# Kernel optimization log

Measured on AMD Instinct MI355X. Metric: run time of the kernel, lower is better.

Reference implementation:

```python
import jax, jax.numpy as jnp
import numpy as np

TAU = 0.7
# Dellar moment flip under x<->y swap: (rho, jy, jx, Pyy, Pxy, Pxx, N, Jy, Jx)
FLIP = np.array([0, 2, 1, 5, 4, 3, 6, 8, 7])


def _dellar_matrices():
    # D2Q9 velocities in lettuce stencil order
    e = np.array([[0, 0], [1, 0], [0, 1], [-1, 0], [0, -1],
                  [1, 1], [-1, 1], [-1, -1], [1, -1]], dtype=np.float64)
    ex, ey = e[:, 0], e[:, 1]
    g = np.array([1, -2, -2, -2, -2, 4, 4, 4, 4], dtype=np.float64)  # Dellar ghost mode
    third = 1.0 / 3.0
    M = np.stack([
        np.ones(9),            # rho
        ex,                    # jx
        ey,                    # jy
        ex * ex - third,       # Pxx - cs^2 rho
        ex * ey,               # Pxy
        ey * ey - third,       # Pyy - cs^2 rho
        g,                     # N (ghost)
        g * ex,                # Jx (ghost)
        g * ey,                # Jy (ghost)
    ])
    return M, np.linalg.inv(M)


def _mlp(x, w1, b1, w2, b2):
    # x: (nx, ny, 9) -> (nx, ny, 1); Linear(9,24) + ReLU + Linear(24,1)
    h = jax.nn.relu(jnp.einsum('xyi,oi->xyo', x, w1) + b1)
    return jnp.einsum('xyo,po->xyp', h, w2) + b2


def setup_inputs() -> dict:
    key = jax.random.key(0)
    ks = jax.random.split(key, 9)
    nx = ny = 2048
    f = jax.random.uniform(ks[0], (9, nx, ny), dtype=jnp.float32)

    def lin_w(k, o, i):
        return jax.random.uniform(k, (o, i), dtype=jnp.float32,
                                  minval=-1.0, maxval=1.0) / np.sqrt(i)

    def lin_b(k, o, i):
        return jax.random.uniform(k, (o,), dtype=jnp.float32,
                                  minval=-1.0, maxval=1.0) / np.sqrt(i)

    M, Minv = _dellar_matrices()
    return {
        'f': f,
        'j_w1': lin_w(ks[1], 24, 9), 'j_b1': lin_b(ks[2], 24, 9),
        'j_w2': lin_w(ks[3], 1, 24), 'j_b2': lin_b(ks[4], 1, 24),
        'n_w1': lin_w(ks[5], 24, 9), 'n_b1': lin_b(ks[6], 24, 9),
        'n_w2': lin_w(ks[7], 1, 24), 'n_b2': lin_b(ks[8], 1, 24),
        'M': jnp.asarray(M, jnp.float32),
        'Minv': jnp.asarray(Minv, jnp.float32),
    }


def reference(f, j_w1, j_b1, j_w2, j_b2, n_w1, n_b1, n_w2, n_b2, M, Minv):
    # moment transform: m_i = M_ij f_j, shape (9, nx, ny)
    m = jnp.einsum('ij,jxy->ixy', M, f)
    mt = jnp.transpose(m, (1, 2, 0))        # (nx, ny, 9)
    mtf = mt[..., FLIP]                     # x<->y flipped moments

    gt_half = lambda a: 0.5 + jnp.exp(a)
    tau_jx = gt_half(_mlp(mt, j_w1, j_b1, j_w2, j_b2))[..., 0]
    tau_jy = gt_half(_mlp(mtf, j_w1, j_b1, j_w2, j_b2))[..., 0]
    tau_n = gt_half(_mlp(mt, n_w1, n_b1, n_w2, n_b2)
                    + _mlp(mtf, n_w1, n_b1, n_w2, n_b2))[..., 0]

    taus = jnp.full_like(m, TAU)
    taus = taus.at[6].set(tau_n).at[7].set(tau_jx).at[8].set(tau_jy)

    rho, jx, jy = m[0], m[1], m[2]
    zero = jnp.zeros_like(rho)
    meq = jnp.stack([rho, jx, jy,
                     jx * jx / rho, jx * jy / rho, jy * jy / rho,
                     zero, zero, zero])

    m_post = m - (m - meq) / taus
    return jnp.einsum('ij,jxy->ixy', Minv, m_post)
```

## Files before the change

### kernel.cpp

```cpp
#include <hip/hip_runtime.h>

typedef float f32x2 __attribute__((ext_vector_type(2)));

__device__ __forceinline__ f32x2 splat2(float s) { f32x2 v; v.x = s; v.y = s; return v; }
__device__ __forceinline__ f32x2 pfmas(float a, f32x2 b, f32x2 c) { return __builtin_elementwise_fma(splat2(a), b, c); }
__device__ __forceinline__ f32x2 prelu(f32x2 a) { return __builtin_elementwise_max(a, splat2(0.0f)); }


__global__ __launch_bounds__(256) void prep_kernel(
    const float* __restrict__ j_w1, const float* __restrict__ j_b1,
    const float* __restrict__ j_w2, const float* __restrict__ j_b2,
    const float* __restrict__ n_w1, const float* __restrict__ n_b1,
    const float* __restrict__ n_w2, const float* __restrict__ n_b2,
    const float* __restrict__ Mg, const float* __restrict__ Minvg,
    float* __restrict__ ws)
{
    const int t = threadIdx.x;
    if (t < 48) {
        const int o = t >> 1, which = t & 1;
        const float* w1 = which ? n_w1 : j_w1;
        const float* b1 = which ? n_b1 : j_b1;
        float w[9];
        #pragma unroll
        for (int i = 0; i < 9; ++i) w[i] = w1[o * 9 + i];
        float* dst = ws + o * 24 + which * 10;
        dst[0] = w[0]; dst[1] = w[4]; dst[2] = w[6];
        dst[3] = 0.5f * (w[1] + w[2]); dst[4] = 0.5f * (w[3] + w[5]); dst[5] = 0.5f * (w[7] + w[8]);
        dst[6] = 0.5f * (w[1] - w[2]); dst[7] = 0.5f * (w[3] - w[5]); dst[8] = 0.5f * (w[7] - w[8]);
        dst[9] = b1[o];
        if (!which) {
            ws[o * 24 + 20] = j_w2[o];
            ws[o * 24 + 21] = n_w2[o];
            ws[o * 24 + 22] = 0.0f;
            ws[o * 24 + 23] = 0.0f;
        }
    } else if (t >= 64 && t < 64 + 81) {
        const int e = t - 64, r = e / 9, i = e % 9;
        float v;
        switch (r) {
            case 0: v = Mg[0 * 9 + i]; break;
            case 1: v = Mg[4 * 9 + i]; break;
            case 2: v = Mg[6 * 9 + i]; break;
            case 3: v = Mg[1 * 9 + i] + Mg[2 * 9 + i]; break;
            case 4: v = Mg[3 * 9 + i] + Mg[5 * 9 + i]; break;
            case 5: v = Mg[7 * 9 + i] + Mg[8 * 9 + i]; break;
            case 6: v = Mg[1 * 9 + i] - Mg[2 * 9 + i]; break;
            case 7: v = Mg[3 * 9 + i] - Mg[5 * 9 + i]; break;
            default: v = Mg[7 * 9 + i] - Mg[8 * 9 + i]; break;
        }
        ws[576 + r * 9 + i] = v;
    } else if (t >= 160 && t < 160 + 54) {
        const int e = t - 160, r = e / 6, c = e % 6;
        ws[672 + e] = -Minvg[r * 9 + 3 + c];
    } else if (t == 254) {
        ws[728] = j_b2[0];
    } else if (t == 255) {
        ws[729] = n_b2[0];
    }
}

__global__ __launch_bounds__(256) void mrt_main(
    const float* __restrict__ f, const float* __restrict__ W,
    float* __restrict__ out, int n2)
{
    long base = ((long)blockIdx.x * 256 + threadIdx.x) * 4;
    if (base + 4 > n2) base = n2 - 4;

    f32x2 fv[2][9];
    f32x2 tv[2][9];
    #pragma unroll
    for (int i = 0; i < 9; ++i) {
        const float4 v = *reinterpret_cast<const float4*>(f + (size_t)i * n2 + base);
        fv[0][i].x = v.x; fv[0][i].y = v.y;
        fv[1][i].x = v.z; fv[1][i].y = v.w;
    }
    #pragma unroll
    for (int r = 0; r < 9; ++r) { tv[0][r] = splat2(0.f); tv[1][r] = splat2(0.f); }
    #pragma unroll
    for (int i = 0; i < 9; ++i) {
        #pragma unroll
        for (int r = 0; r < 9; ++r) {
            const float w = W[576 + r * 9 + i];
            tv[0][r] = pfmas(w, fv[0][i], tv[0][r]);
            tv[1][r] = pfmas(w, fv[1][i], tv[1][r]);
        }
    }

    f32x2 accj[2], accjf[2], accn[2];
    #pragma unroll
    for (int p = 0; p < 2; ++p) { accj[p] = splat2(0.f); accjf[p] = splat2(0.f); accn[p] = splat2(0.f); }

    #pragma unroll 4
    for (int o = 0; o < 24; ++o) {
        const float* wo = W + o * 24;
        const float w0 = wo[0], w1 = wo[1], w2 = wo[2], w3 = wo[3], w4 = wo[4], w5 = wo[5];
        const float a0 = wo[6], a1 = wo[7], a2 = wo[8], b1j = wo[9];
        const float u0 = wo[10], u1 = wo[11], u2 = wo[12], u3 = wo[13], u4 = wo[14], u5 = wo[15];
        const float v0 = wo[16], v1 = wo[17], v2 = wo[18], b1n = wo[19];
        const float w2j = wo[20], w2n = wo[21];
        #pragma unroll
        for (int p = 0; p < 2; ++p) {
            f32x2 s = splat2(b1j);
            s = pfmas(w0, tv[p][0], s);
            s = pfmas(w1, tv[p][1], s);
            s = pfmas(w2, tv[p][2], s);
            s = pfmas(w3, tv[p][3], s);
            s = pfmas(w4, tv[p][4], s);
            s = pfmas(w5, tv[p][5], s);
            f32x2 a = splat2(a0) * tv[p][6];
            a = pfmas(a1, tv[p][7], a);
            a = pfmas(a2, tv[p][8], a);
            accj[p]  = pfmas(w2j, prelu(s + a), accj[p]);
            accjf[p] = pfmas(w2j, prelu(s - a), accjf[p]);

            f32x2 sn = splat2(b1n);
            sn = pfmas(u0, tv[p][0], sn);
            sn = pfmas(u1, tv[p][1], sn);
            sn = pfmas(u2, tv[p][2], sn);
            sn = pfmas(u3, tv[p][3], sn);
            sn = pfmas(u4, tv[p][4], sn);
            sn = pfmas(u5, tv[p][5], sn);
            f32x2 an = splat2(v0) * tv[p][6];
            an = pfmas(v1, tv[p][7], an);
            an = pfmas(v2, tv[p][8], an);
            accn[p] = pfmas(w2n, prelu(sn + an) + prelu(sn - an), accn[p]);
        }
    }

    const float b2j = W[728], b2n = W[729];
    f32x2 d[2][6];
    #pragma unroll
    for (int p = 0; p < 2; ++p) {
        const f32x2 aj  = accj[p]  + splat2(b2j);
        const f32x2 ajf = accjf[p] + splat2(b2j);
        const f32x2 an  = accn[p]  + splat2(2.0f * b2n);
        f32x2 rt7, rt8, rt6, rrho;
        rt7.x = __builtin_amdgcn_rcpf(0.5f + __expf(aj.x));
        rt7.y = __builtin_amdgcn_rcpf(0.5f + __expf(aj.y));
        rt8.x = __builtin_amdgcn_rcpf(0.5f + __expf(ajf.x));
        rt8.y = __builtin_amdgcn_rcpf(0.5f + __expf(ajf.y));
        rt6.x = __builtin_amdgcn_rcpf(0.5f + __expf(an.x));
        rt6.y = __builtin_amdgcn_rcpf(0.5f + __expf(an.y));
        rrho.x = __builtin_amdgcn_rcpf(tv[p][0].x);
        rrho.y = __builtin_amdgcn_rcpf(tv[p][0].y);

        const f32x2 jx = splat2(0.5f) * (tv[p][3] + tv[p][6]);
        const f32x2 jy = splat2(0.5f) * (tv[p][3] - tv[p][6]);
        const f32x2 m3 = splat2(0.5f) * (tv[p][4] + tv[p][7]);
        const f32x2 m5 = splat2(0.5f) * (tv[p][4] - tv[p][7]);
        const f32x2 m7 = splat2(0.5f) * (tv[p][5] + tv[p][8]);
        const f32x2 m8 = splat2(0.5f) * (tv[p][5] - tv[p][8]);
        const f32x2 m4 = tv[p][1], m6 = tv[p][2];

        const f32x2 Cs = splat2(1.0f / 0.7f);
        d[p][0] = (m3 - jx * jx * rrho) * Cs;
        d[p][1] = (m4 - jx * jy * rrho) * Cs;
        d[p][2] = (m5 - jy * jy * rrho) * Cs;
        d[p][3] = m6 * rt6;
        d[p][4] = m7 * rt7;
        d[p][5] = m8 * rt8;
    }

    #pragma unroll
    for (int r = 0; r < 9; ++r) {
        f32x2 o0 = fv[0][r], o1 = fv[1][r];
        #pragma unroll
        for (int c = 0; c < 6; ++c) {
            const float w = W[672 + r * 6 + c];
            o0 = pfmas(w, d[0][c], o0);
            o1 = pfmas(w, d[1][c], o1);
        }
        const float4 vv = make_float4(o0.x, o0.y, o1.x, o1.y);
        *reinterpret_cast<float4*>(out + (size_t)r * n2 + base) = vv;
    }
}

extern "C" void kernel_launch(void* const* d_in, const int* in_sizes, int n_in,
                              void* d_out, int out_size, void* d_ws, size_t ws_size,
                              hipStream_t stream) {
    const float* f    = (const float*)d_in[0];
    const float* j_w1 = (const float*)d_in[1];
    const float* j_b1 = (const float*)d_in[2];
    const float* j_w2 = (const float*)d_in[3];
    const float* j_b2 = (const float*)d_in[4];
    const float* n_w1 = (const float*)d_in[5];
    const float* n_b1 = (const float*)d_in[6];
    const float* n_w2 = (const float*)d_in[7];
    const float* n_b2 = (const float*)d_in[8];
    const float* Mg   = (const float*)d_in[9];
    const float* Minv = (const float*)d_in[10];
    float* out = (float*)d_out;
    float* ws  = (float*)d_ws;

    const int n2 = in_sizes[0] / 9;
    const int pts_per_block = 256 * 4;
    const int grid = (n2 + pts_per_block - 1) / pts_per_block;

    prep_kernel<<<1, 256, 0, stream>>>(j_w1, j_b1, j_w2, j_b2,
                                       n_w1, n_b1, n_w2, n_b2, Mg, Minv, ws);
    mrt_main<<<grid, 256, 0, stream>>>(f, ws, out, n2);
}
```

Before: 303.9 us.

## Use inline packed-FMA asm with SGPR pair weights and eight points per thread

Replaces the compiler-generated packed FMAs with inline v_pk_fma/mul/add asm that reads weight pairs from SGPR pairs through op_sel. This avoids the per-use splat moves of scalar weights. It also doubles the points per thread to 8 and halves the grid. The weight layout is padded to pairs, the last stage now does the full 9-column inverse transform on post-collision moments instead of the 6-column delta update, and the bias and constant handling moves into prep. The costs are higher register pressure with lower occupancy, and the full Minv product adds extra FMAs in the output stage.

```diff
diff --git a/kernel.cpp b/kernel.cpp
--- a/kernel.cpp
+++ b/kernel.cpp
@@ -3,7 +3,39 @@
 typedef float f32x2 __attribute__((ext_vector_type(2)));
 
 __device__ __forceinline__ f32x2 splat2(float s) { f32x2 v; v.x = s; v.y = s; return v; }
-__device__ __forceinline__ f32x2 pfmas(float a, f32x2 b, f32x2 c) { return __builtin_elementwise_fma(splat2(a), b, c); }
+
+__device__ __forceinline__ void pk_fma_l(f32x2& c, const f32x2 w, const f32x2 x) {
+    asm("v_pk_fma_f32 %0, %1, %2, %0 op_sel:[0,0,0] op_sel_hi:[0,1,1]"
+        : "+v"(c) : "s"(w), "v"(x));
+}
+__device__ __forceinline__ void pk_fma_h(f32x2& c, const f32x2 w, const f32x2 x) {
+    asm("v_pk_fma_f32 %0, %1, %2, %0 op_sel:[1,0,0] op_sel_hi:[1,1,1]"
+        : "+v"(c) : "s"(w), "v"(x));
+}
+__device__ __forceinline__ f32x2 pk_mul_l(const f32x2 w, const f32x2 x) {
+    f32x2 d;
+    asm("v_pk_mul_f32 %0, %1, %2 op_sel:[0,0] op_sel_hi:[0,1]"
+        : "=v"(d) : "s"(w), "v"(x));
+    return d;
+}
+__device__ __forceinline__ f32x2 pk_add_l(const f32x2 w, const f32x2 x) {
+    f32x2 d;
+    asm("v_pk_add_f32 %0, %1, %2 op_sel:[0,0] op_sel_hi:[0,1]"
+        : "=v"(d) : "s"(w), "v"(x));
+    return d;
+}
+__device__ __forceinline__ f32x2 pk_add_h(const f32x2 w, const f32x2 x) {
+    f32x2 d;
+    asm("v_pk_add_f32 %0, %1, %2 op_sel:[1,0] op_sel_hi:[1,1]"
+        : "=v"(d) : "s"(w), "v"(x));
+    return d;
+}
+__device__ __forceinline__ f32x2 pk_add(const f32x2 a, const f32x2 b) {
+    f32x2 d;
+    asm("v_pk_add_f32 %0, %1, %2 op_sel:[0,0] op_sel_hi:[1,1]"
+        : "=v"(d) : "v"(a), "v"(b));
+    return d;
+}
 __device__ __forceinline__ f32x2 prelu(f32x2 a) { return __builtin_elementwise_max(a, splat2(0.0f)); }
 
 
@@ -34,10 +66,11 @@
             ws[o * 24 + 22] = 0.0f;
             ws[o * 24 + 23] = 0.0f;
         }
-    } else if (t >= 64 && t < 64 + 81) {
-        const int e = t - 64, r = e / 9, i = e % 9;
+    } else if (t >= 64 && t < 64 + 90) {
+        const int e = t - 64, r = e / 10, i = e % 10;
         float v;
-        switch (r) {
+        if (i == 9) v = 0.0f;
+        else switch (r) {
             case 0: v = Mg[0 * 9 + i]; break;
             case 1: v = Mg[4 * 9 + i]; break;
             case 2: v = Mg[6 * 9 + i]; break;
@@ -48,14 +81,14 @@
             case 7: v = Mg[3 * 9 + i] - Mg[5 * 9 + i]; break;
             default: v = Mg[7 * 9 + i] - Mg[8 * 9 + i]; break;
         }
-        ws[576 + r * 9 + i] = v;
-    } else if (t >= 160 && t < 160 + 54) {
-        const int e = t - 160, r = e / 6, c = e % 6;
-        ws[672 + e] = -Minvg[r * 9 + 3 + c];
+        ws[576 + r * 10 + i] = v;
+    } else if (t >= 160 && t < 160 + 90) {
+        const int e = t - 160, r = e / 10, j = e % 10;
+        ws[672 + r * 10 + j] = (j == 9) ? 0.0f : Minvg[r * 9 + j];
     } else if (t == 254) {
-        ws[728] = j_b2[0];
+        ws[764] = j_b2[0];
     } else if (t == 255) {
-        ws[729] = n_b2[0];
+        ws[765] = 2.0f * n_b2[0];
     }
 }
 
@@ -63,77 +96,90 @@
     const float* __restrict__ f, const float* __restrict__ W,
     float* __restrict__ out, int n2)
 {
-    long base = ((long)blockIdx.x * 256 + threadIdx.x) * 4;
-    if (base + 4 > n2) base = n2 - 4;
-
-    f32x2 fv[2][9];
-    f32x2 tv[2][9];
+    long base = ((long)blockIdx.x * 256 + threadIdx.x) * 8;
+    if (base + 8 > n2) base = n2 - 8;
+
+    f32x2 tv[4][9];
+    {
+        f32x2 fv[4][9];
+        #pragma unroll
+        for (int i = 0; i < 9; ++i) {
+            const float4 u0 = *reinterpret_cast<const float4*>(f + (size_t)i * n2 + base);
+            const float4 u1 = *reinterpret_cast<const float4*>(f + (size_t)i * n2 + base + 4);
+            fv[0][i].x = u0.x; fv[0][i].y = u0.y;
+            fv[1][i].x = u0.z; fv[1][i].y = u0.w;
+            fv[2][i].x = u1.x; fv[2][i].y = u1.y;
+            fv[3][i].x = u1.z; fv[3][i].y = u1.w;
+        }
+        #pragma unroll
+        for (int r = 0; r < 9; ++r) {
+            const f32x2* Tp = reinterpret_cast<const f32x2*>(W + 576 + r * 10);
+            const f32x2 t0 = Tp[0], t1 = Tp[1], t2 = Tp[2], t3 = Tp[3], t4 = Tp[4];
+            #pragma unroll
+            for (int p = 0; p < 4; ++p) {
+                f32x2 acc = pk_mul_l(t0, fv[p][0]);
+                pk_fma_h(acc, t0, fv[p][1]);
+                pk_fma_l(acc, t1, fv[p][2]);
+                pk_fma_h(acc, t1, fv[p][3]);
+                pk_fma_l(acc, t2, fv[p][4]);
+                pk_fma_h(acc, t2, fv[p][5]);
+                pk_fma_l(acc, t3, fv[p][6]);
+                pk_fma_h(acc, t3, fv[p][7]);
+                pk_fma_l(acc, t4, fv[p][8]);
+                tv[p][r] = acc;
+            }
+        }
+    }
+
+    f32x2 accj[4], accjf[4], accn[4];
     #pragma unroll
-    for (int i = 0; i < 9; ++i) {
-        const float4 v = *reinterpret_cast<const float4*>(f + (size_t)i * n2 + base);
-        fv[0][i].x = v.x; fv[0][i].y = v.y;
-        fv[1][i].x = v.z; fv[1][i].y = v.w;
-    }
-    #pragma unroll
-    for (int r = 0; r < 9; ++r) { tv[0][r] = splat2(0.f); tv[1][r] = splat2(0.f); }
-    #pragma unroll
-    for (int i = 0; i < 9; ++i) {
-        #pragma unroll
-        for (int r = 0; r < 9; ++r) {
-            const float w = W[576 + r * 9 + i];
-            tv[0][r] = pfmas(w, fv[0][i], tv[0][r]);
-            tv[1][r] = pfmas(w, fv[1][i], tv[1][r]);
-        }
-    }
-
-    f32x2 accj[2], accjf[2], accn[2];
-    #pragma unroll
-    for (int p = 0; p < 2; ++p) { accj[p] = splat2(0.f); accjf[p] = splat2(0.f); accn[p] = splat2(0.f); }
+    for (int p = 0; p < 4; ++p) { accj[p] = splat2(0.f); accjf[p] = splat2(0.f); accn[p] = splat2(0.f); }
 
     #pragma unroll 4
     for (int o = 0; o < 24; ++o) {
-        const float* wo = W + o * 24;
-        const float w0 = wo[0], w1 = wo[1], w2 = wo[2], w3 = wo[3], w4 = wo[4], w5 = wo[5];
-        const float a0 = wo[6], a1 = wo[7], a2 = wo[8], b1j = wo[9];
-        const float u0 = wo[10], u1 = wo[11], u2 = wo[12], u3 = wo[13], u4 = wo[14], u5 = wo[15];
-        const float v0 = wo[16], v1 = wo[17], v2 = wo[18], b1n = wo[19];
-        const float w2j = wo[20], w2n = wo[21];
-        #pragma unroll
-        for (int p = 0; p < 2; ++p) {
-            f32x2 s = splat2(b1j);
-            s = pfmas(w0, tv[p][0], s);
-            s = pfmas(w1, tv[p][1], s);
-            s = pfmas(w2, tv[p][2], s);
-            s = pfmas(w3, tv[p][3], s);
-            s = pfmas(w4, tv[p][4], s);
-            s = pfmas(w5, tv[p][5], s);
-            f32x2 a = splat2(a0) * tv[p][6];
-            a = pfmas(a1, tv[p][7], a);
-            a = pfmas(a2, tv[p][8], a);
-            accj[p]  = pfmas(w2j, prelu(s + a), accj[p]);
-            accjf[p] = pfmas(w2j, prelu(s - a), accjf[p]);
-
-            f32x2 sn = splat2(b1n);
-            sn = pfmas(u0, tv[p][0], sn);
-            sn = pfmas(u1, tv[p][1], sn);
-            sn = pfmas(u2, tv[p][2], sn);
-            sn = pfmas(u3, tv[p][3], sn);
-            sn = pfmas(u4, tv[p][4], sn);
-            sn = pfmas(u5, tv[p][5], sn);
-            f32x2 an = splat2(v0) * tv[p][6];
-            an = pfmas(v1, tv[p][7], an);
-            an = pfmas(v2, tv[p][8], an);
-            accn[p] = pfmas(w2n, prelu(sn + an) + prelu(sn - an), accn[p]);
-        }
-    }
-
-    const float b2j = W[728], b2n = W[729];
-    f32x2 d[2][6];
+        const f32x2* wp = reinterpret_cast<const f32x2*>(W + o * 24);
+        const f32x2 w01 = wp[0], w23 = wp[1], w45 = wp[2], aa01 = wp[3], a2b = wp[4];
+        const f32x2 u01 = wp[5], u23 = wp[6], u45 = wp[7], vv01 = wp[8], v2b = wp[9];
+        const f32x2 w2p = wp[10];
+        #pragma unroll
+        for (int p = 0; p < 4; ++p) {
+            f32x2 s = pk_mul_l(w01, tv[p][0]);
+            pk_fma_h(s, w01, tv[p][1]);
+            pk_fma_l(s, w23, tv[p][2]);
+            pk_fma_h(s, w23, tv[p][3]);
+            pk_fma_l(s, w45, tv[p][4]);
+            pk_fma_h(s, w45, tv[p][5]);
+            f32x2 a = pk_mul_l(aa01, tv[p][6]);
+            pk_fma_h(a, aa01, tv[p][7]);
+            pk_fma_l(a, a2b, tv[p][8]);
+            const f32x2 hs = prelu(pk_add_h(a2b, pk_add(s, a)));
+            const f32x2 hd = prelu(pk_add_h(a2b, s - a));
+            pk_fma_l(accj[p], w2p, hs);
+            pk_fma_l(accjf[p], w2p, hd);
+
+            f32x2 sn = pk_mul_l(u01, tv[p][0]);
+            pk_fma_h(sn, u01, tv[p][1]);
+            pk_fma_l(sn, u23, tv[p][2]);
+            pk_fma_h(sn, u23, tv[p][3]);
+            pk_fma_l(sn, u45, tv[p][4]);
+            pk_fma_h(sn, u45, tv[p][5]);
+            f32x2 an = pk_mul_l(vv01, tv[p][6]);
+            pk_fma_h(an, vv01, tv[p][7]);
+            pk_fma_l(an, v2b, tv[p][8]);
+            const f32x2 ns = prelu(pk_add_h(v2b, pk_add(sn, an)));
+            const f32x2 nd = prelu(pk_add_h(v2b, sn - an));
+            pk_fma_h(accn[p], w2p, pk_add(ns, nd));
+        }
+    }
+
+    const f32x2 b2p = *reinterpret_cast<const f32x2*>(W + 764);
+    const f32x2 Cs = splat2(1.0f / 0.7f);
+    f32x2 mp[4][9];
     #pragma unroll
-    for (int p = 0; p < 2; ++p) {
-        const f32x2 aj  = accj[p]  + splat2(b2j);
-        const f32x2 ajf = accjf[p] + splat2(b2j);
-        const f32x2 an  = accn[p]  + splat2(2.0f * b2n);
+    for (int p = 0; p < 4; ++p) {
+        const f32x2 aj  = pk_add_l(b2p, accj[p]);
+        const f32x2 ajf = pk_add_l(b2p, accjf[p]);
+        const f32x2 an  = pk_add_h(b2p, accn[p]);
         f32x2 rt7, rt8, rt6, rrho;
         rt7.x = __builtin_amdgcn_rcpf(0.5f + __expf(aj.x));
         rt7.y = __builtin_amdgcn_rcpf(0.5f + __expf(aj.y));
@@ -152,26 +198,39 @@
         const f32x2 m8 = splat2(0.5f) * (tv[p][5] - tv[p][8]);
         const f32x2 m4 = tv[p][1], m6 = tv[p][2];
 
-        const f32x2 Cs = splat2(1.0f / 0.7f);
-        d[p][0] = (m3 - jx * jx * rrho) * Cs;
-        d[p][1] = (m4 - jx * jy * rrho) * Cs;
-        d[p][2] = (m5 - jy * jy * rrho) * Cs;
-        d[p][3] = m6 * rt6;
-        d[p][4] = m7 * rt7;
-        d[p][5] = m8 * rt8;
+        mp[p][0] = tv[p][0];
+        mp[p][1] = jx;
+        mp[p][2] = jy;
+        mp[p][3] = m3 - (m3 - jx * jx * rrho) * Cs;
+        mp[p][4] = m4 - (m4 - jx * jy * rrho) * Cs;
+        mp[p][5] = m5 - (m5 - jy * jy * rrho) * Cs;
+        mp[p][6] = m6 - m6 * rt6;
+        mp[p][7] = m7 - m7 * rt7;
+        mp[p][8] = m8 - m8 * rt8;
     }
 
     #pragma unroll
     for (int r = 0; r < 9; ++r) {
-        f32x2 o0 = fv[0][r], o1 = fv[1][r];
-        #pragma unroll
-        for (int c = 0; c < 6; ++c) {
-            const float w = W[672 + r * 6 + c];
-            o0 = pfmas(w, d[0][c], o0);
-            o1 = pfmas(w, d[1][c], o1);
-        }
-        const float4 vv = make_float4(o0.x, o0.y, o1.x, o1.y);
-        *reinterpret_cast<float4*>(out + (size_t)r * n2 + base) = vv;
+        const f32x2* Qp = reinterpret_cast<const f32x2*>(W + 672 + r * 10);
+        const f32x2 q0 = Qp[0], q1 = Qp[1], q2 = Qp[2], q3 = Qp[3], q4 = Qp[4];
+        f32x2 ov[4];
+        #pragma unroll
+        for (int p = 0; p < 4; ++p) {
+            f32x2 o0 = pk_mul_l(q0, mp[p][0]);
+            pk_fma_h(o0, q0, mp[p][1]);
+            pk_fma_l(o0, q1, mp[p][2]);
+            pk_fma_h(o0, q1, mp[p][3]);
+            pk_fma_l(o0, q2, mp[p][4]);
+            pk_fma_h(o0, q2, mp[p][5]);
+            pk_fma_l(o0, q3, mp[p][6]);
+            pk_fma_h(o0, q3, mp[p][7]);
+            pk_fma_l(o0, q4, mp[p][8]);
+            ov[p] = o0;
+        }
+        const float4 A = make_float4(ov[0].x, ov[0].y, ov[1].x, ov[1].y);
+        const float4 B = make_float4(ov[2].x, ov[2].y, ov[3].x, ov[3].y);
+        *reinterpret_cast<float4*>(out + (size_t)r * n2 + base)     = A;
+        *reinterpret_cast<float4*>(out + (size_t)r * n2 + base + 4) = B;
     }
 }
 
@@ -193,7 +252,7 @@
     float* ws  = (float*)d_ws;
 
     const int n2 = in_sizes[0] / 9;
-    const int pts_per_block = 256 * 4;
+    const int pts_per_block = 256 * 8;
     const int grid = (n2 + pts_per_block - 1) / pts_per_block;
 
     prep_kernel<<<1, 256, 0, stream>>>(j_w1, j_b1, j_w2, j_b2,
```

Result: no change. 308.1 us (+1.4%).

## Run MLP hidden layer in packed fp16 and recompute output via full Minv

Applied to the files above, without the earlier changes.

Moves the two 9→24→1 MLP evaluations from packed fp32 to packed fp16 (v_pk_fma_f16 style), storing splatted half2 weights in the workspace. Inputs to the MLP are converted to half, while the moment transform and collision stay in fp32. The output stage no longer keeps the original f values live; it rebuilds post-collision moments and applies the full 9x9 Minv. This cuts register pressure and MLP ALU cost, but adds nine extra FMAs per output and risks precision loss in the learned relaxation times.

```diff
diff --git a/kernel.cpp b/kernel.cpp
--- a/kernel.cpp
+++ b/kernel.cpp
@@ -1,10 +1,16 @@
 #include <hip/hip_runtime.h>
 
-typedef float f32x2 __attribute__((ext_vector_type(2)));
-
-__device__ __forceinline__ f32x2 splat2(float s) { f32x2 v; v.x = s; v.y = s; return v; }
-__device__ __forceinline__ f32x2 pfmas(float a, f32x2 b, f32x2 c) { return __builtin_elementwise_fma(splat2(a), b, c); }
-__device__ __forceinline__ f32x2 prelu(f32x2 a) { return __builtin_elementwise_max(a, splat2(0.0f)); }
+typedef _Float16 h2 __attribute__((ext_vector_type(2)));
+
+__device__ __forceinline__ h2 h2splat(float s) {
+    const _Float16 v = (_Float16)s;
+    h2 r; r.x = v; r.y = v; return r;
+}
+__device__ __forceinline__ h2 h2fma(h2 a, h2 b, h2 c) { return __builtin_elementwise_fma(a, b, c); }
+__device__ __forceinline__ h2 h2relu(h2 a) {
+    h2 z; z.x = (_Float16)0.0f; z.y = (_Float16)0.0f;
+    return __builtin_elementwise_max(a, z);
+}
 
 
 __global__ __launch_bounds__(256) void prep_kernel(
@@ -16,6 +22,7 @@
     float* __restrict__ ws)
 {
     const int t = threadIdx.x;
+    h2* wh = reinterpret_cast<h2*>(ws);
     if (t < 48) {
         const int o = t >> 1, which = t & 1;
         const float* w1 = which ? n_w1 : j_w1;
@@ -23,16 +30,20 @@
         float w[9];
         #pragma unroll
         for (int i = 0; i < 9; ++i) w[i] = w1[o * 9 + i];
-        float* dst = ws + o * 24 + which * 10;
-        dst[0] = w[0]; dst[1] = w[4]; dst[2] = w[6];
-        dst[3] = 0.5f * (w[1] + w[2]); dst[4] = 0.5f * (w[3] + w[5]); dst[5] = 0.5f * (w[7] + w[8]);
-        dst[6] = 0.5f * (w[1] - w[2]); dst[7] = 0.5f * (w[3] - w[5]); dst[8] = 0.5f * (w[7] - w[8]);
-        dst[9] = b1[o];
+        const int b = o * 22 + which * 10;
+        wh[b + 0] = h2splat(w[0]);
+        wh[b + 1] = h2splat(w[4]);
+        wh[b + 2] = h2splat(w[6]);
+        wh[b + 3] = h2splat(0.5f * (w[1] + w[2]));
+        wh[b + 4] = h2splat(0.5f * (w[3] + w[5]));
+        wh[b + 5] = h2splat(0.5f * (w[7] + w[8]));
+        wh[b + 6] = h2splat(0.5f * (w[1] - w[2]));
+        wh[b + 7] = h2splat(0.5f * (w[3] - w[5]));
+        wh[b + 8] = h2splat(0.5f * (w[7] - w[8]));
+        wh[b + 9] = h2splat(b1[o]);
         if (!which) {
-            ws[o * 24 + 20] = j_w2[o];
-            ws[o * 24 + 21] = n_w2[o];
-            ws[o * 24 + 22] = 0.0f;
-            ws[o * 24 + 23] = 0.0f;
+            wh[o * 22 + 20] = h2splat(j_w2[o]);
+            wh[o * 22 + 21] = h2splat(n_w2[o]);
         }
     } else if (t >= 64 && t < 64 + 81) {
         const int e = t - 64, r = e / 9, i = e % 9;
@@ -48,14 +59,14 @@
             case 7: v = Mg[3 * 9 + i] - Mg[5 * 9 + i]; break;
             default: v = Mg[7 * 9 + i] - Mg[8 * 9 + i]; break;
         }
-        ws[576 + r * 9 + i] = v;
-    } else if (t >= 160 && t < 160 + 54) {
-        const int e = t - 160, r = e / 6, c = e % 6;
-        ws[672 + e] = -Minvg[r * 9 + 3 + c];
+        ws[528 + r * 9 + i] = v;
+    } else if (t >= 160 && t < 160 + 81) {
+        const int e = t - 160;
+        ws[528 + 81 + e] = Minvg[e];
     } else if (t == 254) {
-        ws[728] = j_b2[0];
+        ws[528 + 162] = j_b2[0];
     } else if (t == 255) {
-        ws[729] = n_b2[0];
+        ws[528 + 163] = 2.0f * n_b2[0];
     }
 }
 
@@ -63,114 +74,132 @@
     const float* __restrict__ f, const float* __restrict__ W,
     float* __restrict__ out, int n2)
 {
+    const h2*    Wh = reinterpret_cast<const h2*>(W);
+    const float* Wf = W + 528;
+
     long base = ((long)blockIdx.x * 256 + threadIdx.x) * 4;
     if (base + 4 > n2) base = n2 - 4;
 
-    f32x2 fv[2][9];
-    f32x2 tv[2][9];
-    #pragma unroll
-    for (int i = 0; i < 9; ++i) {
-        const float4 v = *reinterpret_cast<const float4*>(f + (size_t)i * n2 + base);
-        fv[0][i].x = v.x; fv[0][i].y = v.y;
-        fv[1][i].x = v.z; fv[1][i].y = v.w;
-    }
-    #pragma unroll
-    for (int r = 0; r < 9; ++r) { tv[0][r] = splat2(0.f); tv[1][r] = splat2(0.f); }
-    #pragma unroll
-    for (int i = 0; i < 9; ++i) {
+    float tv[9][4];
+    {
+        float fv[9][4];
+        #pragma unroll
+        for (int i = 0; i < 9; ++i) {
+            const float4 u = *reinterpret_cast<const float4*>(f + (size_t)i * n2 + base);
+            fv[i][0] = u.x; fv[i][1] = u.y; fv[i][2] = u.z; fv[i][3] = u.w;
+        }
         #pragma unroll
         for (int r = 0; r < 9; ++r) {
-            const float w = W[576 + r * 9 + i];
-            tv[0][r] = pfmas(w, fv[0][i], tv[0][r]);
-            tv[1][r] = pfmas(w, fv[1][i], tv[1][r]);
-        }
-    }
-
-    f32x2 accj[2], accjf[2], accn[2];
-    #pragma unroll
-    for (int p = 0; p < 2; ++p) { accj[p] = splat2(0.f); accjf[p] = splat2(0.f); accn[p] = splat2(0.f); }
+            float a0 = 0.f, a1 = 0.f, a2 = 0.f, a3 = 0.f;
+            #pragma unroll
+            for (int i = 0; i < 9; ++i) {
+                const float w = Wf[r * 9 + i];
+                a0 = fmaf(w, fv[i][0], a0);
+                a1 = fmaf(w, fv[i][1], a1);
+                a2 = fmaf(w, fv[i][2], a2);
+                a3 = fmaf(w, fv[i][3], a3);
+            }
+            tv[r][0] = a0; tv[r][1] = a1; tv[r][2] = a2; tv[r][3] = a3;
+        }
+    }
+
+    h2 tvh[9][2];
+    #pragma unroll
+    for (int r = 0; r < 9; ++r) {
+        tvh[r][0].x = (_Float16)tv[r][0]; tvh[r][0].y = (_Float16)tv[r][1];
+        tvh[r][1].x = (_Float16)tv[r][2]; tvh[r][1].y = (_Float16)tv[r][3];
+    }
+
+    h2 accj[2], accjf[2], accn[2];
+    #pragma unroll
+    for (int p = 0; p < 2; ++p) { accj[p] = h2splat(0.f); accjf[p] = h2splat(0.f); accn[p] = h2splat(0.f); }
 
     #pragma unroll 4
     for (int o = 0; o < 24; ++o) {
-        const float* wo = W + o * 24;
-        const float w0 = wo[0], w1 = wo[1], w2 = wo[2], w3 = wo[3], w4 = wo[4], w5 = wo[5];
-        const float a0 = wo[6], a1 = wo[7], a2 = wo[8], b1j = wo[9];
-        const float u0 = wo[10], u1 = wo[11], u2 = wo[12], u3 = wo[13], u4 = wo[14], u5 = wo[15];
-        const float v0 = wo[16], v1 = wo[17], v2 = wo[18], b1n = wo[19];
-        const float w2j = wo[20], w2n = wo[21];
+        const h2 s0 = Wh[o*22+0], s1 = Wh[o*22+1], s2 = Wh[o*22+2];
+        const h2 s3 = Wh[o*22+3], s4 = Wh[o*22+4], s5 = Wh[o*22+5];
+        const h2 a0 = Wh[o*22+6], a1 = Wh[o*22+7], a2 = Wh[o*22+8];
+        const h2 b1j = Wh[o*22+9];
+        const h2 u0 = Wh[o*22+10], u1 = Wh[o*22+11], u2 = Wh[o*22+12];
+        const h2 u3 = Wh[o*22+13], u4 = Wh[o*22+14], u5 = Wh[o*22+15];
+        const h2 v0 = Wh[o*22+16], v1 = Wh[o*22+17], v2 = Wh[o*22+18];
+        const h2 b1n = Wh[o*22+19];
+        const h2 w2j = Wh[o*22+20], w2n = Wh[o*22+21];
         #pragma unroll
         for (int p = 0; p < 2; ++p) {
-            f32x2 s = splat2(b1j);
-            s = pfmas(w0, tv[p][0], s);
-            s = pfmas(w1, tv[p][1], s);
-            s = pfmas(w2, tv[p][2], s);
-            s = pfmas(w3, tv[p][3], s);
-            s = pfmas(w4, tv[p][4], s);
-            s = pfmas(w5, tv[p][5], s);
-            f32x2 a = splat2(a0) * tv[p][6];
-            a = pfmas(a1, tv[p][7], a);
-            a = pfmas(a2, tv[p][8], a);
-            accj[p]  = pfmas(w2j, prelu(s + a), accj[p]);
-            accjf[p] = pfmas(w2j, prelu(s - a), accjf[p]);
-
-            f32x2 sn = splat2(b1n);
-            sn = pfmas(u0, tv[p][0], sn);
-            sn = pfmas(u1, tv[p][1], sn);
-            sn = pfmas(u2, tv[p][2], sn);
-            sn = pfmas(u3, tv[p][3], sn);
-            sn = pfmas(u4, tv[p][4], sn);
-            sn = pfmas(u5, tv[p][5], sn);
-            f32x2 an = splat2(v0) * tv[p][6];
-            an = pfmas(v1, tv[p][7], an);
-            an = pfmas(v2, tv[p][8], an);
-            accn[p] = pfmas(w2n, prelu(sn + an) + prelu(sn - an), accn[p]);
-        }
-    }
-
-    const float b2j = W[728], b2n = W[729];
-    f32x2 d[2][6];
-    #pragma unroll
-    for (int p = 0; p < 2; ++p) {
-        const f32x2 aj  = accj[p]  + splat2(b2j);
-        const f32x2 ajf = accjf[p] + splat2(b2j);
-        const f32x2 an  = accn[p]  + splat2(2.0f * b2n);
-        f32x2 rt7, rt8, rt6, rrho;
-        rt7.x = __builtin_amdgcn_rcpf(0.5f + __expf(aj.x));
-        rt7.y = __builtin_amdgcn_rcpf(0.5f + __expf(aj.y));
-        rt8.x = __builtin_amdgcn_rcpf(0.5f + __expf(ajf.x));
-        rt8.y = __builtin_amdgcn_rcpf(0.5f + __expf(ajf.y));
-        rt6.x = __builtin_amdgcn_rcpf(0.5f + __expf(an.x));
-        rt6.y = __builtin_amdgcn_rcpf(0.5f + __expf(an.y));
-        rrho.x = __builtin_amdgcn_rcpf(tv[p][0].x);
-        rrho.y = __builtin_amdgcn_rcpf(tv[p][0].y);
-
-        const f32x2 jx = splat2(0.5f) * (tv[p][3] + tv[p][6]);
-        const f32x2 jy = splat2(0.5f) * (tv[p][3] - tv[p][6]);
-        const f32x2 m3 = splat2(0.5f) * (tv[p][4] + tv[p][7]);
-        const f32x2 m5 = splat2(0.5f) * (tv[p][4] - tv[p][7]);
-        const f32x2 m7 = splat2(0.5f) * (tv[p][5] + tv[p][8]);
-        const f32x2 m8 = splat2(0.5f) * (tv[p][5] - tv[p][8]);
-        const f32x2 m4 = tv[p][1], m6 = tv[p][2];
-
-        const f32x2 Cs = splat2(1.0f / 0.7f);
-        d[p][0] = (m3 - jx * jx * rrho) * Cs;
-        d[p][1] = (m4 - jx * jy * rrho) * Cs;
-        d[p][2] = (m5 - jy * jy * rrho) * Cs;
-        d[p][3] = m6 * rt6;
-        d[p][4] = m7 * rt7;
-        d[p][5] = m8 * rt8;
+            h2 s = h2fma(s0, tvh[0][p], b1j);
+            s = h2fma(s1, tvh[1][p], s);
+            s = h2fma(s2, tvh[2][p], s);
+            s = h2fma(s3, tvh[3][p], s);
+            s = h2fma(s4, tvh[4][p], s);
+            s = h2fma(s5, tvh[5][p], s);
+            h2 a = a0 * tvh[6][p];
+            a = h2fma(a1, tvh[7][p], a);
+            a = h2fma(a2, tvh[8][p], a);
+            const h2 hs = h2relu(s + a);
+            const h2 hd = h2relu(s - a);
+            accj[p]  = h2fma(w2j, hs, accj[p]);
+            accjf[p] = h2fma(w2j, hd, accjf[p]);
+
+            h2 sn = h2fma(u0, tvh[0][p], b1n);
+            sn = h2fma(u1, tvh[1][p], sn);
+            sn = h2fma(u2, tvh[2][p], sn);
+            sn = h2fma(u3, tvh[3][p], sn);
+            sn = h2fma(u4, tvh[4][p], sn);
+            sn = h2fma(u5, tvh[5][p], sn);
+            h2 an = v0 * tvh[6][p];
+            an = h2fma(v1, tvh[7][p], an);
+            an = h2fma(v2, tvh[8][p], an);
+            const h2 ns = h2relu(sn + an);
+            const h2 nd = h2relu(sn - an);
+            accn[p] = h2fma(w2n, ns + nd, accn[p]);
+        }
+    }
+
+    const float b2j = Wf[162], b2n2 = Wf[163];
+    const float Cs = 1.0f / 0.7f;
+    #pragma unroll
+    for (int k = 0; k < 4; ++k) {
+        const int p = k >> 1;
+        const float aj  = (k & 1) ? (float)accj[p].y  : (float)accj[p].x;
+        const float ajf = (k & 1) ? (float)accjf[p].y : (float)accjf[p].x;
+        const float an  = (k & 1) ? (float)accn[p].y  : (float)accn[p].x;
+
+        const float rt7 = __builtin_amdgcn_rcpf(0.5f + __expf(aj + b2j));
+        const float rt8 = __builtin_amdgcn_rcpf(0.5f + __expf(ajf + b2j));
+        const float rt6 = __builtin_amdgcn_rcpf(0.5f + __expf(an + b2n2));
+        const float rrho = __builtin_amdgcn_rcpf(tv[0][k]);
+
+        const float jx = 0.5f * (tv[3][k] + tv[6][k]);
+        const float jy = 0.5f * (tv[3][k] - tv[6][k]);
+        const float m3 = 0.5f * (tv[4][k] + tv[7][k]);
+        const float m5 = 0.5f * (tv[4][k] - tv[7][k]);
+        const float m7 = 0.5f * (tv[5][k] + tv[8][k]);
+        const float m8 = 0.5f * (tv[5][k] - tv[8][k]);
+        const float m4 = tv[1][k], m6 = tv[2][k];
+
+        tv[1][k] = jx;
+        tv[2][k] = jy;
+        tv[3][k] = m3 - (m3 - jx * jx * rrho) * Cs;
+        tv[4][k] = m4 - (m4 - jx * jy * rrho) * Cs;
+        tv[5][k] = m5 - (m5 - jy * jy * rrho) * Cs;
+        tv[6][k] = m6 - m6 * rt6;
+        tv[7][k] = m7 - m7 * rt7;
+        tv[8][k] = m8 - m8 * rt8;
     }
 
     #pragma unroll
     for (int r = 0; r < 9; ++r) {
-        f32x2 o0 = fv[0][r], o1 = fv[1][r];
-        #pragma unroll
-        for (int c = 0; c < 6; ++c) {
-            const float w = W[672 + r * 6 + c];
-            o0 = pfmas(w, d[0][c], o0);
-            o1 = pfmas(w, d[1][c], o1);
-        }
-        const float4 vv = make_float4(o0.x, o0.y, o1.x, o1.y);
+        float o0 = 0.f, o1 = 0.f, o2 = 0.f, o3 = 0.f;
+        #pragma unroll
+        for (int j = 0; j < 9; ++j) {
+            const float w = Wf[81 + r * 9 + j];
+            o0 = fmaf(w, tv[j][0], o0);
+            o1 = fmaf(w, tv[j][1], o1);
+            o2 = fmaf(w, tv[j][2], o2);
+            o3 = fmaf(w, tv[j][3], o3);
+        }
+        const float4 vv = make_float4(o0, o1, o2, o3);
         *reinterpret_cast<float4*>(out + (size_t)r * n2 + base) = vv;
     }
 }
```

After: 295.7 us. -2.7%, faster.
